# Optimization experiments

Hardware: AMD Instinct MI355X
Metric: run time of the kernel (lower is better)

Reference implementation:

```python
import jax, jax.numpy as jnp
import numpy as np
from jax.scipy.special import logsumexp

SENT_LEN = 4194304
LABELS = 2

def setup_inputs() -> dict:
    key = jax.random.key(0)
    k1, k2 = jax.random.split(key)
    feats = jax.random.normal(k1, (SENT_LEN, LABELS), dtype=jnp.float32)
    transitions = jax.random.normal(k2, (LABELS, LABELS), dtype=jnp.float32)
    return {"feats": feats, "transitions": transitions}

def reference(feats, transitions):
    # Linear-chain CRF marginals for a single sentence (batch=1), label_size=2.
    # alpha[0] = feats[0]; alpha[i][n] = feats[i,n] + LSE_p(alpha[i-1][p] + T[n,p])
    def fwd_step(alpha, f):
        a = f + logsumexp(alpha[None, :] + transitions, axis=1)
        return a, a
    a0 = feats[0]
    _, alphas_rest = jax.lax.scan(fwd_step, a0, feats[1:])
    alpha = jnp.concatenate([a0[None], alphas_rest], axis=0)  # [L, 2]
    Z1 = logsumexp(alpha[-1])

    # beta[L-1] = feats[L-1]; beta[i][p] = feats[i,p] + LSE_n(beta[i+1][n] + T[n,p])
    def bwd_step(beta, f):
        b = f + logsumexp(beta[:, None] + transitions, axis=0)
        return b, b
    bT = feats[-1]
    _, betas_rest = jax.lax.scan(bwd_step, bT, feats[:-1][::-1])
    beta = jnp.concatenate([bT[None], betas_rest], axis=0)[::-1]  # [L, 2]

    # message = alpha + beta - feats (emission double-counted); marginal = exp(message - Z)
    marginal = jnp.exp(alpha + beta - feats - Z1)
    return marginal
```

## Files before the change

### kernel.cpp

```cpp
#include <hip/hip_runtime.h>


#define N_LEN    4194304
#define SC       16
#define NC       (N_LEN / SC)
#define NG       (NC / 64)
#define K1_BLOCK 256
#define K2_T     1024
#define K2_G     (NG / K2_T)
#define K3_CPB   256
#define K3_TILE  (K3_CPB * SC)
#define LROW     33

__device__ __forceinline__ double lse2d(double x, double y) {
    double mx = fmax(x, y);
    double d  = fmin(x, y) - mx;
    float  cc = __logf(1.0f + __expf((float)d));
    return mx + (double)cc;
}

struct DMat { double m00, m01, m10, m11; };

__device__ __forceinline__ DMat logmm(const DMat X, const DMat Y) {
    DMat R;
    R.m00 = lse2d(X.m00 + Y.m00, X.m01 + Y.m10);
    R.m01 = lse2d(X.m00 + Y.m01, X.m01 + Y.m11);
    R.m10 = lse2d(X.m10 + Y.m00, X.m11 + Y.m10);
    R.m11 = lse2d(X.m10 + Y.m01, X.m11 + Y.m11);
    return R;
}

__device__ __forceinline__ DMat shfl_up_mat(const DMat M, int off) {
    DMat R;
    R.m00 = __shfl_up(M.m00, off, 64);
    R.m01 = __shfl_up(M.m01, off, 64);
    R.m10 = __shfl_up(M.m10, off, 64);
    R.m11 = __shfl_up(M.m11, off, 64);
    return R;
}

__device__ __forceinline__ DMat shfl_down_mat(const DMat M, int off) {
    DMat R;
    R.m00 = __shfl_down(M.m00, off, 64);
    R.m01 = __shfl_down(M.m01, off, 64);
    R.m10 = __shfl_down(M.m10, off, 64);
    R.m11 = __shfl_down(M.m11, off, 64);
    return R;
}

__global__ __launch_bounds__(K1_BLOCK, 4) void crf_k1(
    const float* __restrict__ feats, const float* __restrict__ trans,
    DMat* __restrict__ PF, DMat* __restrict__ SB,
    DMat* __restrict__ GF, DMat* __restrict__ GB)
{
    const int c    = blockIdx.x * blockDim.x + threadIdx.x;
    const int lane = threadIdx.x & 63;
    const int g    = c >> 6;
    const double t00 = trans[0], t01 = trans[1], t10 = trans[2], t11 = trans[3];

    const int lo_f = c * SC + 1;
    const int hi_f = min((c + 1) * SC, N_LEN - 1);
    const int lo_b = max(c * SC - 1, 0);
    const int hi_b = (c + 1) * SC - 2;

    DMat F, B;
    for (int j = lo_b; j <= hi_f; ++j) {
        float2 f = *(const float2*)(feats + 2 * j);
        const double fx = f.x, fy = f.y;
        if (j == lo_b) {
            B.m00 = fx + t00; B.m01 = fx + t10;
            B.m10 = fy + t01; B.m11 = fy + t11;
        } else if (j <= hi_b) {
            double b00 = fx + t00, b01 = fx + t10;
            double b10 = fy + t01, b11 = fy + t11;
            double n00 = lse2d(B.m00 + b00, B.m01 + b10);
            double n01 = lse2d(B.m00 + b01, B.m01 + b11);
            double n10 = lse2d(B.m10 + b00, B.m11 + b10);
            double n11 = lse2d(B.m10 + b01, B.m11 + b11);
            B.m00 = n00; B.m01 = n01; B.m10 = n10; B.m11 = n11;
        }
        if (j == lo_f) {
            F.m00 = fx + t00; F.m01 = fx + t01;
            F.m10 = fy + t10; F.m11 = fy + t11;
        } else if (j > lo_f && j <= hi_f) {
            double l0 = lse2d(t00 + F.m00, t01 + F.m10);
            double l1 = lse2d(t00 + F.m01, t01 + F.m11);
            double l2 = lse2d(t10 + F.m00, t11 + F.m10);
            double l3 = lse2d(t10 + F.m01, t11 + F.m11);
            F.m00 = fx + l0; F.m01 = fx + l1;
            F.m10 = fy + l2; F.m11 = fy + l3;
        }
    }

    DMat S = F;
    #pragma unroll
    for (int k = 0; k < 6; ++k) {
        int off = 1 << k;
        DMat o = shfl_up_mat(S, off);
        if (lane >= off) S = logmm(S, o);
    }
    PF[c] = S;
    if (lane == 63) GF[g] = S;

    DMat T = B;
    #pragma unroll
    for (int k = 0; k < 6; ++k) {
        int off = 1 << k;
        DMat o = shfl_down_mat(T, off);
        if (lane + off < 64) T = logmm(T, o);
    }
    SB[c] = T;
    if (lane == 0) GB[g] = T;
}

__global__ __launch_bounds__(K2_T) void crf_k2(
    const float* __restrict__ feats,
    const DMat* __restrict__ GF, const DMat* __restrict__ GB,
    double2* __restrict__ gstart, double2* __restrict__ gend,
    double* __restrict__ zout)
{
    __shared__ DMat sm[K2_T];
    const int t  = threadIdx.x;
    const int c0 = t * K2_G;

    if (blockIdx.x == 0) {
        DMat M = GF[c0];
        #pragma unroll
        for (int k = 1; k < K2_G; ++k) M = logmm(GF[c0 + k], M);
        sm[t] = M;
        __syncthreads();
        for (int off = 1; off < K2_T; off <<= 1) {
            DMat R; bool act = (t >= off);
            if (act) R = logmm(sm[t], sm[t - off]);
            __syncthreads();
            if (act) sm[t] = R;
            __syncthreads();
        }
        float2 f0 = *(const float2*)feats;
        double v0, v1;
        if (t == 0) { v0 = f0.x; v1 = f0.y; }
        else {
            DMat E = sm[t - 1];
            v0 = lse2d(E.m00 + (double)f0.x, E.m01 + (double)f0.y);
            v1 = lse2d(E.m10 + (double)f0.x, E.m11 + (double)f0.y);
        }
        #pragma unroll
        for (int k = 0; k < K2_G; ++k) {
            int c = c0 + k;
            gstart[c] = make_double2(v0, v1);
            DMat P = GF[c];
            double n0 = lse2d(P.m00 + v0, P.m01 + v1);
            double n1 = lse2d(P.m10 + v0, P.m11 + v1);
            v0 = n0; v1 = n1;
        }
        if (t == K2_T - 1) zout[0] = lse2d(v0, v1);
    } else {
        DMat M = GB[c0];
        #pragma unroll
        for (int k = 1; k < K2_G; ++k) M = logmm(M, GB[c0 + k]);
        sm[t] = M;
        __syncthreads();
        for (int off = 1; off < K2_T; off <<= 1) {
            DMat R; bool act = (t + off < K2_T);
            if (act) R = logmm(sm[t], sm[t + off]);
            __syncthreads();
            if (act) sm[t] = R;
            __syncthreads();
        }
        float2 fl = *(const float2*)(feats + 2 * (N_LEN - 1));
        double w0, w1;
        if (t == K2_T - 1) { w0 = fl.x; w1 = fl.y; }
        else {
            DMat E = sm[t + 1];
            w0 = lse2d(E.m00 + (double)fl.x, E.m01 + (double)fl.y);
            w1 = lse2d(E.m10 + (double)fl.x, E.m11 + (double)fl.y);
        }
        #pragma unroll
        for (int k = K2_G - 1; k >= 0; --k) {
            int c = c0 + k;
            gend[c] = make_double2(w0, w1);
            DMat Q = GB[c];
            double n0 = lse2d(Q.m00 + w0, Q.m01 + w1);
            double n1 = lse2d(Q.m10 + w0, Q.m11 + w1);
            w0 = n0; w1 = n1;
        }
    }
}

__global__ __launch_bounds__(K3_CPB, 4) void crf_k3(
    const float* __restrict__ feats, const float* __restrict__ trans,
    const DMat* __restrict__ PF, const DMat* __restrict__ SB,
    const double2* __restrict__ gstart, const double2* __restrict__ gend,
    const double* __restrict__ zptr, float* __restrict__ out)
{
    __shared__ float lds[K3_CPB * LROW];
    const int t = threadIdx.x;
    const int c = blockIdx.x * K3_CPB + t;
    const int g = c >> 6, r = c & 63;
    const int tile = blockIdx.x * K3_TILE;
    const double t00 = trans[0], t01 = trans[1], t10 = trans[2], t11 = trans[3];
    const double Z = zptr[0];
    const float2* fv = (const float2*)feats;

    #pragma unroll
    for (int k = 0; k < SC; ++k) {
        int p = k * K3_CPB + t;
        float2 f = fv[tile + p];
        int cc = p >> 4, ii = p & 15;
        lds[cc * LROW + 2 * ii]     = f.x;
        lds[cc * LROW + 2 * ii + 1] = f.y;
    }

    double2 gs = gstart[g], ge = gend[g];
    double2 v, w;
    if (r == 0) {
        v = gs;
    } else {
        DMat P = PF[c - 1];
        v = make_double2(lse2d(P.m00 + gs.x, P.m01 + gs.y),
                         lse2d(P.m10 + gs.x, P.m11 + gs.y));
    }
    if (r == 63) {
        w = ge;
    } else {
        DMat Tm = SB[c + 1];
        w = make_double2(lse2d(Tm.m00 + ge.x, Tm.m01 + ge.y),
                         lse2d(Tm.m10 + ge.x, Tm.m11 + ge.y));
    }
    __syncthreads();

    const float* myrow = lds + t * LROW;
    float* myroww = lds + t * LROW;

    float bx[SC], by[SC];
    const double base = w.x;
    bx[SC - 1] = 0.0f;
    by[SC - 1] = (float)(w.y - base);
    #pragma unroll
    for (int k = SC - 2; k >= 0; --k) {
        double fx = (double)myrow[2 * k], fy = (double)myrow[2 * k + 1];
        double n0 = fx + lse2d(t00 + w.x, t10 + w.y);
        double n1 = fy + lse2d(t01 + w.x, t11 + w.y);
        w.x = n0; w.y = n1;
        bx[k] = (float)(w.x - base);
        by[k] = (float)(w.y - base);
    }

    const double zb = Z - base;
    #pragma unroll
    for (int k = 0; k < SC; ++k) {
        float fxf = myrow[2 * k], fyf = myrow[2 * k + 1];
        if (k > 0) {
            double n0 = (double)fxf + lse2d(t00 + v.x, t01 + v.y);
            double n1 = (double)fyf + lse2d(t10 + v.x, t11 + v.y);
            v.x = n0; v.y = n1;
        }
        float m0 = (float)((v.x - zb) + (double)(bx[k] - fxf));
        float m1 = (float)((v.y - zb) + (double)(by[k] - fyf));
        myroww[2 * k]     = __expf(m0);
        myroww[2 * k + 1] = __expf(m1);
    }
    __syncthreads();

    float2* ov = (float2*)out;
    #pragma unroll
    for (int k = 0; k < SC; ++k) {
        int p = k * K3_CPB + t;
        int cc = p >> 4, ii = p & 15;
        ov[tile + p] = make_float2(lds[cc * LROW + 2 * ii],
                                   lds[cc * LROW + 2 * ii + 1]);
    }
}

extern "C" void kernel_launch(void* const* d_in, const int* in_sizes, int n_in,
                              void* d_out, int out_size, void* d_ws, size_t ws_size,
                              hipStream_t stream)
{
    const float* feats = (const float*)d_in[0];
    const float* trans = (const float*)d_in[1];
    float* out = (float*)d_out;

    char* ws = (char*)d_ws;
    size_t off = 0;
    DMat* PF = (DMat*)(ws + off); off += (size_t)NC * sizeof(DMat);
    DMat* SB = (DMat*)(ws + off); off += (size_t)NC * sizeof(DMat);
    DMat* GF = (DMat*)(ws + off); off += (size_t)NG * sizeof(DMat);
    DMat* GB = (DMat*)(ws + off); off += (size_t)NG * sizeof(DMat);
    double2* gstart = (double2*)(ws + off); off += (size_t)NG * sizeof(double2);
    double2* gend   = (double2*)(ws + off); off += (size_t)NG * sizeof(double2);
    double*  zout   = (double*)(ws + off);

    hipLaunchKernelGGL(crf_k1, dim3(NC / K1_BLOCK), dim3(K1_BLOCK), 0, stream,
                       feats, trans, PF, SB, GF, GB);
    hipLaunchKernelGGL(crf_k2, dim3(2), dim3(K2_T), 0, stream,
                       feats, GF, GB, gstart, gend, zout);
    hipLaunchKernelGGL(crf_k3, dim3(NC / K3_CPB), dim3(K3_CPB), 0, stream,
                       feats, trans, PF, SB, gstart, gend, zout, out);
}
```

Baseline: 156.4 us.

## Use fp32 chunk recurrences, block-level scan, and fp32 prefix storage

```diff
diff --git a/kernel.cpp b/kernel.cpp
--- a/kernel.cpp
+++ b/kernel.cpp
@@ -4,13 +4,16 @@
 #define N_LEN    4194304
 #define SC       16
 #define NC       (N_LEN / SC)
-#define NG       (NC / 64)
-#define K1_BLOCK 256
+#define CPB      256
+#define NG       (NC / CPB)
 #define K2_T     1024
-#define K2_G     (NG / K2_T)
-#define K3_CPB   256
-#define K3_TILE  (K3_CPB * SC)
 #define LROW     33
+
+__device__ __forceinline__ float lse2f(float x, float y) {
+    float mx = fmaxf(x, y);
+    float d  = fminf(x, y) - mx;
+    return mx + __logf(1.0f + __expf(d));
+}
 
 __device__ __forceinline__ double lse2d(double x, double y) {
     double mx = fmax(x, y);
@@ -20,6 +23,7 @@
 }
 
 struct DMat { double m00, m01, m10, m11; };
+struct FMat { float  m00, m01, m10, m11; };
 
 __device__ __forceinline__ DMat logmm(const DMat X, const DMat Y) {
     DMat R;
@@ -48,69 +52,85 @@
     return R;
 }
 
-__global__ __launch_bounds__(K1_BLOCK, 4) void crf_k1(
+__global__ __launch_bounds__(CPB, 4) void crf_k1(
     const float* __restrict__ feats, const float* __restrict__ trans,
-    DMat* __restrict__ PF, DMat* __restrict__ SB,
+    FMat* __restrict__ PF, FMat* __restrict__ SB,
     DMat* __restrict__ GF, DMat* __restrict__ GB)
 {
     const int c    = blockIdx.x * blockDim.x + threadIdx.x;
     const int lane = threadIdx.x & 63;
-    const int g    = c >> 6;
-    const double t00 = trans[0], t01 = trans[1], t10 = trans[2], t11 = trans[3];
+    const int wv   = threadIdx.x >> 6;
+    const float t00 = trans[0], t01 = trans[1], t10 = trans[2], t11 = trans[3];
 
     const int lo_f = c * SC + 1;
     const int hi_f = min((c + 1) * SC, N_LEN - 1);
     const int lo_b = max(c * SC - 1, 0);
     const int hi_b = (c + 1) * SC - 2;
 
-    DMat F, B;
+    FMat F, B;
     for (int j = lo_b; j <= hi_f; ++j) {
         float2 f = *(const float2*)(feats + 2 * j);
-        const double fx = f.x, fy = f.y;
+        const float fx = f.x, fy = f.y;
         if (j == lo_b) {
             B.m00 = fx + t00; B.m01 = fx + t10;
             B.m10 = fy + t01; B.m11 = fy + t11;
         } else if (j <= hi_b) {
-            double b00 = fx + t00, b01 = fx + t10;
-            double b10 = fy + t01, b11 = fy + t11;
-            double n00 = lse2d(B.m00 + b00, B.m01 + b10);
-            double n01 = lse2d(B.m00 + b01, B.m01 + b11);
-            double n10 = lse2d(B.m10 + b00, B.m11 + b10);
-            double n11 = lse2d(B.m10 + b01, B.m11 + b11);
+            float b00 = fx + t00, b01 = fx + t10;
+            float b10 = fy + t01, b11 = fy + t11;
+            float n00 = lse2f(B.m00 + b00, B.m01 + b10);
+            float n01 = lse2f(B.m00 + b01, B.m01 + b11);
+            float n10 = lse2f(B.m10 + b00, B.m11 + b10);
+            float n11 = lse2f(B.m10 + b01, B.m11 + b11);
             B.m00 = n00; B.m01 = n01; B.m10 = n10; B.m11 = n11;
         }
         if (j == lo_f) {
             F.m00 = fx + t00; F.m01 = fx + t01;
             F.m10 = fy + t10; F.m11 = fy + t11;
         } else if (j > lo_f && j <= hi_f) {
-            double l0 = lse2d(t00 + F.m00, t01 + F.m10);
-            double l1 = lse2d(t00 + F.m01, t01 + F.m11);
-            double l2 = lse2d(t10 + F.m00, t11 + F.m10);
-            double l3 = lse2d(t10 + F.m01, t11 + F.m11);
+            float l0 = lse2f(t00 + F.m00, t01 + F.m10);
+            float l1 = lse2f(t00 + F.m01, t01 + F.m11);
+            float l2 = lse2f(t10 + F.m00, t11 + F.m10);
+            float l3 = lse2f(t10 + F.m01, t11 + F.m11);
             F.m00 = fx + l0; F.m01 = fx + l1;
             F.m10 = fy + l2; F.m11 = fy + l3;
         }
     }
 
-    DMat S = F;
+    DMat S = { (double)F.m00, (double)F.m01, (double)F.m10, (double)F.m11 };
+    DMat T = { (double)B.m00, (double)B.m01, (double)B.m10, (double)B.m11 };
+
     #pragma unroll
     for (int k = 0; k < 6; ++k) {
         int off = 1 << k;
         DMat o = shfl_up_mat(S, off);
         if (lane >= off) S = logmm(S, o);
     }
-    PF[c] = S;
-    if (lane == 63) GF[g] = S;
-
-    DMat T = B;
     #pragma unroll
     for (int k = 0; k < 6; ++k) {
         int off = 1 << k;
         DMat o = shfl_down_mat(T, off);
         if (lane + off < 64) T = logmm(T, o);
     }
-    SB[c] = T;
-    if (lane == 0) GB[g] = T;
+
+    __shared__ DMat wp[4], sb[4];
+    if (lane == 63) wp[wv] = S;
+    if (lane == 0)  sb[wv] = T;
+    __syncthreads();
+    if (wv > 0) {
+        DMat Pre = wp[0];
+        for (int u = 1; u < wv; ++u) Pre = logmm(wp[u], Pre);
+        S = logmm(S, Pre);
+    }
+    if (wv < 3) {
+        DMat Suf = sb[3];
+        for (int u = 2; u > wv; --u) Suf = logmm(sb[u], Suf);
+        T = logmm(T, Suf);
+    }
+
+    PF[c] = { (float)S.m00, (float)S.m01, (float)S.m10, (float)S.m11 };
+    SB[c] = { (float)T.m00, (float)T.m01, (float)T.m10, (float)T.m11 };
+    if (wv == 3 && lane == 63) GF[blockIdx.x] = S;
+    if (wv == 0 && lane == 0)  GB[blockIdx.x] = T;
 }
 
 __global__ __launch_bounds__(K2_T) void crf_k2(
@@ -119,92 +139,79 @@
     double2* __restrict__ gstart, double2* __restrict__ gend,
     double* __restrict__ zout)
 {
-    __shared__ DMat sm[K2_T];
-    const int t  = threadIdx.x;
-    const int c0 = t * K2_G;
+    __shared__ double s00[K2_T], s01[K2_T], s10[K2_T], s11[K2_T];
+    const int t = threadIdx.x;
 
     if (blockIdx.x == 0) {
-        DMat M = GF[c0];
-        #pragma unroll
-        for (int k = 1; k < K2_G; ++k) M = logmm(GF[c0 + k], M);
-        sm[t] = M;
+        DMat M = GF[t];
+        s00[t] = M.m00; s01[t] = M.m01; s10[t] = M.m10; s11[t] = M.m11;
         __syncthreads();
         for (int off = 1; off < K2_T; off <<= 1) {
-            DMat R; bool act = (t >= off);
-            if (act) R = logmm(sm[t], sm[t - off]);
+            if (t >= off) {
+                DMat O = { s00[t-off], s01[t-off], s10[t-off], s11[t-off] };
+                M = logmm(M, O);
+            }
             __syncthreads();
-            if (act) sm[t] = R;
+            s00[t] = M.m00; s01[t] = M.m01; s10[t] = M.m10; s11[t] = M.m11;
             __syncthreads();
         }
         float2 f0 = *(const float2*)feats;
-        double v0, v1;
-        if (t == 0) { v0 = f0.x; v1 = f0.y; }
-        else {
-            DMat E = sm[t - 1];
-            v0 = lse2d(E.m00 + (double)f0.x, E.m01 + (double)f0.y);
-            v1 = lse2d(E.m10 + (double)f0.x, E.m11 + (double)f0.y);
-        }
-        #pragma unroll
-        for (int k = 0; k < K2_G; ++k) {
-            int c = c0 + k;
-            gstart[c] = make_double2(v0, v1);
-            DMat P = GF[c];
-            double n0 = lse2d(P.m00 + v0, P.m01 + v1);
-            double n1 = lse2d(P.m10 + v0, P.m11 + v1);
-            v0 = n0; v1 = n1;
-        }
-        if (t == K2_T - 1) zout[0] = lse2d(v0, v1);
+        if (t == 0) {
+            gstart[0] = make_double2((double)f0.x, (double)f0.y);
+        } else {
+            DMat E = { s00[t-1], s01[t-1], s10[t-1], s11[t-1] };
+            gstart[t] = make_double2(
+                lse2d(E.m00 + (double)f0.x, E.m01 + (double)f0.y),
+                lse2d(E.m10 + (double)f0.x, E.m11 + (double)f0.y));
+        }
+        if (t == K2_T - 1) {
+            double a0 = lse2d(M.m00 + (double)f0.x, M.m01 + (double)f0.y);
+            double a1 = lse2d(M.m10 + (double)f0.x, M.m11 + (double)f0.y);
+            zout[0] = lse2d(a0, a1);
+        }
     } else {
-        DMat M = GB[c0];
-        #pragma unroll
-        for (int k = 1; k < K2_G; ++k) M = logmm(M, GB[c0 + k]);
-        sm[t] = M;
+        DMat M = GB[t];
+        s00[t] = M.m00; s01[t] = M.m01; s10[t] = M.m10; s11[t] = M.m11;
         __syncthreads();
         for (int off = 1; off < K2_T; off <<= 1) {
-            DMat R; bool act = (t + off < K2_T);
-            if (act) R = logmm(sm[t], sm[t + off]);
+            if (t + off < K2_T) {
+                DMat O = { s00[t+off], s01[t+off], s10[t+off], s11[t+off] };
+                M = logmm(M, O);
+            }
             __syncthreads();
-            if (act) sm[t] = R;
+            s00[t] = M.m00; s01[t] = M.m01; s10[t] = M.m10; s11[t] = M.m11;
             __syncthreads();
         }
         float2 fl = *(const float2*)(feats + 2 * (N_LEN - 1));
-        double w0, w1;
-        if (t == K2_T - 1) { w0 = fl.x; w1 = fl.y; }
-        else {
-            DMat E = sm[t + 1];
-            w0 = lse2d(E.m00 + (double)fl.x, E.m01 + (double)fl.y);
-            w1 = lse2d(E.m10 + (double)fl.x, E.m11 + (double)fl.y);
-        }
-        #pragma unroll
-        for (int k = K2_G - 1; k >= 0; --k) {
-            int c = c0 + k;
-            gend[c] = make_double2(w0, w1);
-            DMat Q = GB[c];
-            double n0 = lse2d(Q.m00 + w0, Q.m01 + w1);
-            double n1 = lse2d(Q.m10 + w0, Q.m11 + w1);
-            w0 = n0; w1 = n1;
-        }
-    }
-}
-
-__global__ __launch_bounds__(K3_CPB, 4) void crf_k3(
+        if (t == K2_T - 1) {
+            gend[t] = make_double2((double)fl.x, (double)fl.y);
+        } else {
+            DMat E = { s00[t+1], s01[t+1], s10[t+1], s11[t+1] };
+            gend[t] = make_double2(
+                lse2d(E.m00 + (double)fl.x, E.m01 + (double)fl.y),
+                lse2d(E.m10 + (double)fl.x, E.m11 + (double)fl.y));
+        }
+    }
+}
+
+__global__ __launch_bounds__(CPB, 4) void crf_k3(
     const float* __restrict__ feats, const float* __restrict__ trans,
-    const DMat* __restrict__ PF, const DMat* __restrict__ SB,
+    const FMat* __restrict__ PF, const FMat* __restrict__ SB,
     const double2* __restrict__ gstart, const double2* __restrict__ gend,
     const double* __restrict__ zptr, float* __restrict__ out)
 {
-    __shared__ float lds[K3_CPB * LROW];
+    __shared__ float lds[CPB * LROW];
     const int t = threadIdx.x;
-    const int c = blockIdx.x * K3_CPB + t;
-    const int g = c >> 6, r = c & 63;
-    const int tile = blockIdx.x * K3_TILE;
-    const double t00 = trans[0], t01 = trans[1], t10 = trans[2], t11 = trans[3];
+    const int c = blockIdx.x * CPB + t;
+    const int g = c >> 8, r = c & 255;
+    const int tile = blockIdx.x * (CPB * SC);
+    const float t00 = trans[0], t01 = trans[1], t10 = trans[2], t11 = trans[3];
     const double Z = zptr[0];
     const float2* fv = (const float2*)feats;
 
     #pragma unroll
     for (int k = 0; k < SC; ++k) {
-        int p = k * K3_CPB + t;
+        int p = k * CPB + t;
         float2 f = fv[tile + p];
         int cc = p >> 4, ii = p & 15;
         lds[cc * LROW + 2 * ii]     = f.x;
@@ -216,47 +223,48 @@
     if (r == 0) {
         v = gs;
     } else {
-        DMat P = PF[c - 1];
-        v = make_double2(lse2d(P.m00 + gs.x, P.m01 + gs.y),
-                         lse2d(P.m10 + gs.x, P.m11 + gs.y));
-    }
-    if (r == 63) {
+        FMat P = PF[c - 1];
+        v = make_double2(lse2d((double)P.m00 + gs.x, (double)P.m01 + gs.y),
+                         lse2d((double)P.m10 + gs.x, (double)P.m11 + gs.y));
+    }
+    if (r == 255) {
         w = ge;
     } else {
-        DMat Tm = SB[c + 1];
-        w = make_double2(lse2d(Tm.m00 + ge.x, Tm.m01 + ge.y),
-                         lse2d(Tm.m10 + ge.x, Tm.m11 + ge.y));
+        FMat Tm = SB[c + 1];
+        w = make_double2(lse2d((double)Tm.m00 + ge.x, (double)Tm.m01 + ge.y),
+                         lse2d((double)Tm.m10 + ge.x, (double)Tm.m11 + ge.y));
     }
     __syncthreads();
 
     const float* myrow = lds + t * LROW;
     float* myroww = lds + t * LROW;
 
+    const double wbase = w.x;
+    float w0 = 0.0f, w1 = (float)(w.y - wbase);
     float bx[SC], by[SC];
-    const double base = w.x;
-    bx[SC - 1] = 0.0f;
-    by[SC - 1] = (float)(w.y - base);
+    bx[SC - 1] = w0; by[SC - 1] = w1;
     #pragma unroll
     for (int k = SC - 2; k >= 0; --k) {
-        double fx = (double)myrow[2 * k], fy = (double)myrow[2 * k + 1];
-        double n0 = fx + lse2d(t00 + w.x, t10 + w.y);
-        double n1 = fy + lse2d(t01 + w.x, t11 + w.y);
-        w.x = n0; w.y = n1;
-        bx[k] = (float)(w.x - base);
-        by[k] = (float)(w.y - base);
-    }
-
-    const double zb = Z - base;
+        float fx = myrow[2 * k], fy = myrow[2 * k + 1];
+        float n0 = fx + lse2f(t00 + w0, t10 + w1);
+        float n1 = fy + lse2f(t01 + w0, t11 + w1);
+        w0 = n0; w1 = n1;
+        bx[k] = w0; by[k] = w1;
+    }
+
+    const double vbase = v.x;
+    float a0 = 0.0f, a1 = (float)(v.y - vbase);
+    const float cbase = (float)((vbase + wbase) - Z);
     #pragma unroll
     for (int k = 0; k < SC; ++k) {
-        float fxf = myrow[2 * k], fyf = myrow[2 * k + 1];
+        float fx = myrow[2 * k], fy = myrow[2 * k + 1];
         if (k > 0) {
-            double n0 = (double)fxf + lse2d(t00 + v.x, t01 + v.y);
-            double n1 = (double)fyf + lse2d(t10 + v.x, t11 + v.y);
-            v.x = n0; v.y = n1;
-        }
-        float m0 = (float)((v.x - zb) + (double)(bx[k] - fxf));
-        float m1 = (float)((v.y - zb) + (double)(by[k] - fyf));
+            float n0 = fx + lse2f(t00 + a0, t01 + a1);
+            float n1 = fy + lse2f(t10 + a0, t11 + a1);
+            a0 = n0; a1 = n1;
+        }
+        float m0 = cbase + a0 + bx[k] - fx;
+        float m1 = cbase + a1 + by[k] - fy;
         myroww[2 * k]     = __expf(m0);
         myroww[2 * k + 1] = __expf(m1);
     }
@@ -265,7 +273,7 @@
     float2* ov = (float2*)out;
     #pragma unroll
     for (int k = 0; k < SC; ++k) {
-        int p = k * K3_CPB + t;
+        int p = k * CPB + t;
         int cc = p >> 4, ii = p & 15;
         ov[tile + p] = make_float2(lds[cc * LROW + 2 * ii],
                                    lds[cc * LROW + 2 * ii + 1]);
@@ -282,18 +290,18 @@
 
     char* ws = (char*)d_ws;
     size_t off = 0;
-    DMat* PF = (DMat*)(ws + off); off += (size_t)NC * sizeof(DMat);
-    DMat* SB = (DMat*)(ws + off); off += (size_t)NC * sizeof(DMat);
+    FMat* PF = (FMat*)(ws + off); off += (size_t)NC * sizeof(FMat);
+    FMat* SB = (FMat*)(ws + off); off += (size_t)NC * sizeof(FMat);
     DMat* GF = (DMat*)(ws + off); off += (size_t)NG * sizeof(DMat);
     DMat* GB = (DMat*)(ws + off); off += (size_t)NG * sizeof(DMat);
     double2* gstart = (double2*)(ws + off); off += (size_t)NG * sizeof(double2);
     double2* gend   = (double2*)(ws + off); off += (size_t)NG * sizeof(double2);
     double*  zout   = (double*)(ws + off);
 
-    hipLaunchKernelGGL(crf_k1, dim3(NC / K1_BLOCK), dim3(K1_BLOCK), 0, stream,
+    hipLaunchKernelGGL(crf_k1, dim3(NC / CPB), dim3(CPB), 0, stream,
                        feats, trans, PF, SB, GF, GB);
     hipLaunchKernelGGL(crf_k2, dim3(2), dim3(K2_T), 0, stream,
                        feats, GF, GB, gstart, gend, zout);
-    hipLaunchKernelGGL(crf_k3, dim3(NC / K3_CPB), dim3(K3_CPB), 0, stream,
+    hipLaunchKernelGGL(crf_k3, dim3(NC / CPB), dim3(CPB), 0, stream,
                        feats, trans, PF, SB, gstart, gend, zout, out);
 }
```

Result: faster. 137.7 us (-11.9%).
